# Kernel tuning notes

Measured on AMD Instinct MI355X. Metric: run time of the kernel, lower is better.

Reference implementation:

```python
import jax, jax.numpy as jnp
import numpy as np

EMBED_DIM = 1024
SEQ_LEN = 2048
BATCH = 4


def setup_inputs() -> dict:
    key = jax.random.key(0)
    kx, kq, kk, kv = jax.random.split(key, 4)
    scale = 1.0 / np.sqrt(EMBED_DIM)
    x = jax.random.normal(kx, (BATCH, SEQ_LEN, EMBED_DIM), dtype=jnp.float32)
    # nn.Linear weights are [out, in]; stored transposed-application here
    W_query = jax.random.normal(kq, (EMBED_DIM, EMBED_DIM), dtype=jnp.float32) * scale
    W_key = jax.random.normal(kk, (EMBED_DIM, EMBED_DIM), dtype=jnp.float32) * scale
    W_value = jax.random.normal(kv, (EMBED_DIM, EMBED_DIM), dtype=jnp.float32) * scale
    return {"x": x, "W_query": W_query, "W_key": W_key, "W_value": W_value}


def reference(x, W_query, W_key, W_value):
    # x: [B, S, D]; W_*: [D_out, D_in] (torch nn.Linear layout -> y = x @ W.T)
    B, S, D = x.shape
    q = jnp.einsum("bsd,ed->bse", x, W_query)
    k = jnp.einsum("bsd,ed->bse", x, W_key)
    v = jnp.einsum("bsd,ed->bse", x, W_value)
    scores = jnp.einsum("bqd,bkd->bqk", q, k)  # [B, S, S]
    causal = jnp.triu(jnp.ones((S, S), dtype=bool), k=1)  # True above diagonal
    scores = jnp.where(causal, -jnp.inf, scores)
    weights = jax.nn.softmax(scores / jnp.sqrt(jnp.asarray(D, x.dtype)), axis=-1)
    return jnp.einsum("bqk,bkd->bqd", weights, v)
```

## Files before the change

### kernel.cpp

```cpp
#include <hip/hip_runtime.h>
#include <stdint.h>

typedef __bf16 bf16_t;
typedef __bf16 bf16x8 __attribute__((ext_vector_type(8)));
typedef float  f32x4  __attribute__((ext_vector_type(4)));

#define AS1 __attribute__((address_space(1)))
#define AS3 __attribute__((address_space(3)))

__device__ __forceinline__ void gld_lds16(const bf16_t* g, void* s) {
  __builtin_amdgcn_global_load_lds((const AS1 uint32_t*)g, (AS3 uint32_t*)s, 16, 0, 0);
}

__global__ __launch_bounds__(256) void convert_all_kernel(
    const float* __restrict__ X,  const float* __restrict__ Wq,
    const float* __restrict__ Wk, const float* __restrict__ Wv,
    bf16_t* __restrict__ Xc, bf16_t* __restrict__ Wqc,
    bf16_t* __restrict__ Wkc, bf16_t* __restrict__ Wvc) {
  const int blk = blockIdx.x;
  const float* src; bf16_t* dst; int base;
  if (blk < 4096)      { src = X;  dst = Xc;  base = 0;    }
  else if (blk < 4608) { src = Wq; dst = Wqc; base = 4096; }
  else if (blk < 5120) { src = Wk; dst = Wkc; base = 4608; }
  else                 { src = Wv; dst = Wvc; base = 5120; }
  const int i = ((blk - base) * 256 + threadIdx.x) * 8;
  const float4 a = ((const float4*)(src + i))[0];
  const float4 b = ((const float4*)(src + i))[1];
  bf16x8 v;
  v[0] = (bf16_t)a.x; v[1] = (bf16_t)a.y; v[2] = (bf16_t)a.z; v[3] = (bf16_t)a.w;
  v[4] = (bf16_t)b.x; v[5] = (bf16_t)b.y; v[6] = (bf16_t)b.z; v[7] = (bf16_t)b.w;
  *(bf16x8*)(dst + i) = v;
}

__device__ __forceinline__ void gemm_bt_core(
    const bf16_t* __restrict__ A, int lda,
    const bf16_t* __restrict__ B, int ldb,
    int m0, int n0, int kBeg, int kEnd,
    bf16_t* As, bf16_t* Bs, f32x4 acc[4][4])
{
  const int tid  = threadIdx.x;
  const int lane = tid & 63;
  const int wave = tid >> 6;
  const int wm = (wave >> 1) * 64;
  const int wn = (wave & 1) * 64;
  const int fr = lane & 15;
  const int ck = lane >> 4;

  const int off0 = wave * 2048 + lane * 16;
  const int row0 = wave * 32 + (lane >> 2);
  const int row1 = row0 + 16;
  const int kg   = ((lane & 3) ^ ((row0 >> 1) & 3)) * 8;

  int aoff[4], boff[4];
#pragma unroll
  for (int i = 0; i < 4; ++i) {
    const int ra = wm + i * 16 + fr;
    const int rb = wn + i * 16 + fr;
    aoff[i] = ra * 64 + ((ck ^ ((ra >> 1) & 3)) * 16);
    boff[i] = rb * 64 + ((ck ^ ((rb >> 1) & 3)) * 16);
  }

  for (int kt = kBeg; kt < kEnd; kt += 32) {
    __syncthreads();
    gld_lds16(A + (size_t)(m0 + row0) * lda + kt + kg, (char*)As + off0);
    gld_lds16(A + (size_t)(m0 + row1) * lda + kt + kg, (char*)As + off0 + 1024);
    gld_lds16(B + (size_t)(n0 + row0) * ldb + kt + kg, (char*)Bs + off0);
    gld_lds16(B + (size_t)(n0 + row1) * ldb + kt + kg, (char*)Bs + off0 + 1024);
    __syncthreads();

    bf16x8 af[4], bfv[4];
#pragma unroll
    for (int mi = 0; mi < 4; ++mi)
      af[mi] = *(const bf16x8*)((char*)As + aoff[mi]);
#pragma unroll
    for (int ni = 0; ni < 4; ++ni)
      bfv[ni] = *(const bf16x8*)((char*)Bs + boff[ni]);
#pragma unroll
    for (int mi = 0; mi < 4; ++mi)
#pragma unroll
      for (int ni = 0; ni < 4; ++ni)
        acc[mi][ni] = __builtin_amdgcn_mfma_f32_16x16x32_bf16(
            af[mi], bfv[ni], acc[mi][ni], 0, 0, 0);
  }
}

__global__ __launch_bounds__(256) void qkv_kernel(
    const bf16_t* __restrict__ X,
    const bf16_t* __restrict__ Wq, const bf16_t* __restrict__ Wk,
    const bf16_t* __restrict__ Wv,
    bf16_t* __restrict__ Q, bf16_t* __restrict__ K, bf16_t* __restrict__ V)
{
  __shared__ bf16_t As[128 * 32];
  __shared__ bf16_t Bs[128 * 32];
  const int m0 = blockIdx.x * 128;
  const int n0 = blockIdx.y * 128;
  const int z  = blockIdx.z;
  const bf16_t* W = (z == 0) ? Wq : (z == 1) ? Wk : Wv;
  bf16_t* Out     = (z == 0) ? Q  : (z == 1) ? K  : V;

  f32x4 acc[4][4] = {};
  gemm_bt_core(X, 1024, W, 1024, m0, n0, 0, 1024, As, Bs, acc);

  const int lane = threadIdx.x & 63;
  const int wave = threadIdx.x >> 6;
  const int wm = (wave >> 1) * 64, wn = (wave & 1) * 64;
#pragma unroll
  for (int mi = 0; mi < 4; ++mi)
#pragma unroll
    for (int r = 0; r < 4; ++r) {
      const int row = m0 + wm + mi * 16 + (lane >> 4) * 4 + r;
#pragma unroll
      for (int ni = 0; ni < 4; ++ni) {
        const int col = n0 + wn + ni * 16 + (lane & 15);
        Out[(size_t)row * 1024 + col] = (bf16_t)acc[mi][ni][r];
      }
    }
}

__global__ __launch_bounds__(256) void vt_kernel(
    const bf16_t* __restrict__ V, bf16_t* __restrict__ Vt)
{
  __shared__ bf16_t t[64][66];
  const int b  = blockIdx.z;
  const int s0 = blockIdx.x * 64;
  const int d0 = blockIdx.y * 64;
  const bf16_t* Vb = V  + (size_t)b * 2048 * 1024;
  bf16_t* Vtb      = Vt + (size_t)b * 1024 * 2048;
  const int c = threadIdx.x & 63, r4 = threadIdx.x >> 6;
#pragma unroll
  for (int i = 0; i < 16; ++i) {
    const int r = r4 + i * 4;
    t[r][c] = Vb[(size_t)(s0 + r) * 1024 + d0 + c];
  }
  __syncthreads();
#pragma unroll
  for (int i = 0; i < 16; ++i) {
    const int r = r4 + i * 4;
    Vtb[(size_t)(d0 + r) * 2048 + s0 + c] = t[c][r];
  }
}

__global__ __launch_bounds__(256) void scores_exp_kernel(
    const bf16_t* __restrict__ Q, const bf16_t* __restrict__ K,
    bf16_t* __restrict__ P, float* __restrict__ partials)
{
  const int kt = blockIdx.x;
  const int mt = blockIdx.y;
  if (kt > mt) return;
  const int m0 = mt * 128;
  const int n0 = kt * 128;
  __shared__ bf16_t As[128 * 32];
  __shared__ bf16_t Bs[128 * 32];
  __shared__ float rowsum[2][128];
  const int batch = blockIdx.z;
  const bf16_t* Qb = Q + (size_t)batch * 2048 * 1024;
  const bf16_t* Kb = K + (size_t)batch * 2048 * 1024;
  bf16_t* Pb = P + (size_t)batch * 2048 * 2048;
  float* lp  = partials + ((size_t)batch * 16 + kt) * 2048;

  f32x4 acc[4][4] = {};
  gemm_bt_core(Qb, 1024, Kb, 1024, m0, n0, 0, 1024, As, Bs, acc);

  const int lane = threadIdx.x & 63;
  const int wave = threadIdx.x >> 6;
  const int wm = (wave >> 1) * 64, wn = (wave & 1) * 64;
  const float c = 0.04508422f;
#pragma unroll
  for (int mi = 0; mi < 4; ++mi)
#pragma unroll
    for (int r = 0; r < 4; ++r) {
      const int lrow = wm + mi * 16 + (lane >> 4) * 4 + r;
      const int row  = m0 + lrow;
      float rs = 0.f;
#pragma unroll
      for (int ni = 0; ni < 4; ++ni) {
        const int col = n0 + wn + ni * 16 + (lane & 15);
        float p = exp2f(acc[mi][ni][r] * c);
        if (col > row) p = 0.f;
        const bf16_t pb = (bf16_t)p;
        Pb[(size_t)row * 2048 + col] = pb;
        rs += (float)pb;
      }
      rs += __shfl_xor(rs, 1);
      rs += __shfl_xor(rs, 2);
      rs += __shfl_xor(rs, 4);
      rs += __shfl_xor(rs, 8);
      if ((lane & 15) == 0) rowsum[wave & 1][lrow] = rs;
    }
  __syncthreads();
  if (threadIdx.x < 128)
    lp[m0 + threadIdx.x] = rowsum[0][threadIdx.x] + rowsum[1][threadIdx.x];
}

__global__ __launch_bounds__(256) void lsum_kernel(
    const float* __restrict__ partials, float* __restrict__ Linv)
{
  const int id  = blockIdx.x * 256 + threadIdx.x;
  const int z   = id >> 11;
  const int row = id & 2047;
  const float* lp = partials + (size_t)z * 16 * 2048;
  const int tmax = row >> 7;
  float l = 0.f;
  for (int kt = 0; kt <= tmax; ++kt) l += lp[kt * 2048 + row];
  Linv[id] = 1.f / l;
}

__global__ __launch_bounds__(256) void pv_kernel(
    const bf16_t* __restrict__ P, const bf16_t* __restrict__ Vt,
    const float* __restrict__ Linv, float* __restrict__ out)
{
  __shared__ bf16_t As[128 * 32];
  __shared__ bf16_t Bs[128 * 32];
  const int zb = blockIdx.z;
  const int mt = ((zb >> 1) & 1) ? (15 - blockIdx.y) : blockIdx.y;
  const int m0 = mt * 128;
  const int n0 = blockIdx.x * 128;
  const bf16_t* Pb  = P  + (size_t)zb * 2048 * 2048;
  const bf16_t* Vtb = Vt + (size_t)zb * 1024 * 2048;
  const float* li = Linv + (size_t)zb * 2048;
  float* ob = out + (size_t)zb * 2048 * 1024;

  f32x4 acc[4][4] = {};
  gemm_bt_core(Pb, 2048, Vtb, 2048, m0, n0, 0, m0 + 128, As, Bs, acc);

  const int lane = threadIdx.x & 63;
  const int wave = threadIdx.x >> 6;
  const int wm = (wave >> 1) * 64, wn = (wave & 1) * 64;
#pragma unroll
  for (int mi = 0; mi < 4; ++mi)
#pragma unroll
    for (int r = 0; r < 4; ++r) {
      const int row = m0 + wm + mi * 16 + (lane >> 4) * 4 + r;
      const float inv = li[row];
#pragma unroll
      for (int ni = 0; ni < 4; ++ni) {
        const int col = n0 + wn + ni * 16 + (lane & 15);
        ob[(size_t)row * 1024 + col] = acc[mi][ni][r] * inv;
      }
    }
}

extern "C" void kernel_launch(void* const* d_in, const int* in_sizes, int n_in,
                              void* d_out, int out_size, void* d_ws, size_t ws_size,
                              hipStream_t stream) {
  const float* X  = (const float*)d_in[0];
  const float* Wq = (const float*)d_in[1];
  const float* Wk = (const float*)d_in[2];
  const float* Wv = (const float*)d_in[3];
  float* out = (float*)d_out;
  char* ws = (char*)d_ws;

  const size_t MB = 1024 * 1024;
  bf16_t* Q    = (bf16_t*)(ws + 0 * MB);
  bf16_t* K    = (bf16_t*)(ws + 16 * MB);
  bf16_t* V    = (bf16_t*)(ws + 32 * MB);
  bf16_t* Xc   = (bf16_t*)(ws + 48 * MB);
  bf16_t* Wqc  = (bf16_t*)(ws + 64 * MB);
  bf16_t* Wkc  = (bf16_t*)(ws + 66 * MB);
  bf16_t* Wvc  = (bf16_t*)(ws + 68 * MB);
  bf16_t* P    = (bf16_t*)(ws + 48 * MB);
  bf16_t* Vt   = (bf16_t*)(ws + 0 * MB);
  float*  Lp   = (float*)(ws + 80 * MB);
  float*  Linv = (float*)(ws + 80 * MB + 512 * 1024);

  convert_all_kernel<<<dim3(5632), 256, 0, stream>>>(X, Wq, Wk, Wv, Xc, Wqc, Wkc, Wvc);
  qkv_kernel<<<dim3(64, 8, 3), 256, 0, stream>>>(Xc, Wqc, Wkc, Wvc, Q, K, V);
  scores_exp_kernel<<<dim3(16, 16, 4), 256, 0, stream>>>(Q, K, P, Lp);
  lsum_kernel<<<dim3(32), 256, 0, stream>>>(Lp, Linv);
  vt_kernel<<<dim3(32, 16, 4), 256, 0, stream>>>(V, Vt);
  pv_kernel<<<dim3(8, 16, 4), 256, 0, stream>>>(P, Vt, Linv, out);
}
```

Baseline: 265.2 us.

## Double GEMM K-tile to 64 and fuse V transpose into QKV epilogue

The shared GEMM core now stages 64-wide K tiles with an 8-way XOR swizzle, halving the number of barrier pairs per K loop and issuing more MFMAs per synchronization. The QKV kernel writes V directly in transposed layout through an LDS staging buffer, which removes the separate vt_kernel launch and its extra read and write of V. This doubles the LDS footprint per block, which may reduce occupancy, and adds extra barriers in the V epilogue.

```diff
diff --git a/kernel.cpp b/kernel.cpp
--- a/kernel.cpp
+++ b/kernel.cpp
@@ -2,6 +2,7 @@
 #include <stdint.h>
 
 typedef __bf16 bf16_t;
+typedef __bf16 bf16x4 __attribute__((ext_vector_type(4)));
 typedef __bf16 bf16x8 __attribute__((ext_vector_type(8)));
 typedef float  f32x4  __attribute__((ext_vector_type(4)));
 
@@ -38,49 +39,62 @@
     int m0, int n0, int kBeg, int kEnd,
     bf16_t* As, bf16_t* Bs, f32x4 acc[4][4])
 {
-  const int tid  = threadIdx.x;
-  const int lane = tid & 63;
-  const int wave = tid >> 6;
+  const int lane = threadIdx.x & 63;
+  const int wave = threadIdx.x >> 6;
   const int wm = (wave >> 1) * 64;
   const int wn = (wave & 1) * 64;
   const int fr = lane & 15;
   const int ck = lane >> 4;
 
-  const int off0 = wave * 2048 + lane * 16;
-  const int row0 = wave * 32 + (lane >> 2);
-  const int row1 = row0 + 16;
-  const int kg   = ((lane & 3) ^ ((row0 >> 1) & 3)) * 8;
-
-  int aoff[4], boff[4];
+  const int srow = lane >> 3;
+  const int sch  = lane & 7;
+
+  int grow[4], kg[4], dst[4];
+#pragma unroll
+  for (int j = 0; j < 4; ++j) {
+    const int r = wave * 32 + j * 8 + srow;
+    grow[j] = r;
+    kg[j]   = (sch ^ (r & 7)) * 8;
+    dst[j]  = r * 128 + sch * 16;
+  }
+
+  int aoff[4][2], boff[4][2];
 #pragma unroll
   for (int i = 0; i < 4; ++i) {
     const int ra = wm + i * 16 + fr;
     const int rb = wn + i * 16 + fr;
-    aoff[i] = ra * 64 + ((ck ^ ((ra >> 1) & 3)) * 16);
-    boff[i] = rb * 64 + ((ck ^ ((rb >> 1) & 3)) * 16);
-  }
-
-  for (int kt = kBeg; kt < kEnd; kt += 32) {
+#pragma unroll
+    for (int kh = 0; kh < 2; ++kh) {
+      aoff[i][kh] = ra * 128 + (((kh * 4 + ck) ^ (ra & 7)) * 16);
+      boff[i][kh] = rb * 128 + (((kh * 4 + ck) ^ (rb & 7)) * 16);
+    }
+  }
+
+  for (int kt = kBeg; kt < kEnd; kt += 64) {
     __syncthreads();
-    gld_lds16(A + (size_t)(m0 + row0) * lda + kt + kg, (char*)As + off0);
-    gld_lds16(A + (size_t)(m0 + row1) * lda + kt + kg, (char*)As + off0 + 1024);
-    gld_lds16(B + (size_t)(n0 + row0) * ldb + kt + kg, (char*)Bs + off0);
-    gld_lds16(B + (size_t)(n0 + row1) * ldb + kt + kg, (char*)Bs + off0 + 1024);
+#pragma unroll
+    for (int j = 0; j < 4; ++j) {
+      gld_lds16(A + (size_t)(m0 + grow[j]) * lda + kt + kg[j], (char*)As + dst[j]);
+      gld_lds16(B + (size_t)(n0 + grow[j]) * ldb + kt + kg[j], (char*)Bs + dst[j]);
+    }
     __syncthreads();
 
-    bf16x8 af[4], bfv[4];
-#pragma unroll
-    for (int mi = 0; mi < 4; ++mi)
-      af[mi] = *(const bf16x8*)((char*)As + aoff[mi]);
-#pragma unroll
-    for (int ni = 0; ni < 4; ++ni)
-      bfv[ni] = *(const bf16x8*)((char*)Bs + boff[ni]);
-#pragma unroll
-    for (int mi = 0; mi < 4; ++mi)
-#pragma unroll
-      for (int ni = 0; ni < 4; ++ni)
-        acc[mi][ni] = __builtin_amdgcn_mfma_f32_16x16x32_bf16(
-            af[mi], bfv[ni], acc[mi][ni], 0, 0, 0);
+    bf16x8 af[4][2], bfv[4][2];
+#pragma unroll
+    for (int i = 0; i < 4; ++i)
+#pragma unroll
+      for (int kh = 0; kh < 2; ++kh) {
+        af[i][kh]  = *(const bf16x8*)((char*)As + aoff[i][kh]);
+        bfv[i][kh] = *(const bf16x8*)((char*)Bs + boff[i][kh]);
+      }
+#pragma unroll
+    for (int kh = 0; kh < 2; ++kh)
+#pragma unroll
+      for (int mi = 0; mi < 4; ++mi)
+#pragma unroll
+        for (int ni = 0; ni < 4; ++ni)
+          acc[mi][ni] = __builtin_amdgcn_mfma_f32_16x16x32_bf16(
+              af[mi][kh], bfv[ni][kh], acc[mi][ni], 0, 0, 0);
   }
 }
 
@@ -88,15 +102,15 @@
     const bf16_t* __restrict__ X,
     const bf16_t* __restrict__ Wq, const bf16_t* __restrict__ Wk,
     const bf16_t* __restrict__ Wv,
-    bf16_t* __restrict__ Q, bf16_t* __restrict__ K, bf16_t* __restrict__ V)
-{
-  __shared__ bf16_t As[128 * 32];
-  __shared__ bf16_t Bs[128 * 32];
+    bf16_t* __restrict__ Q, bf16_t* __restrict__ K, bf16_t* __restrict__ Vt)
+{
+  __shared__ bf16_t smem[2 * 128 * 64];
+  bf16_t* As = smem;
+  bf16_t* Bs = smem + 128 * 64;
   const int m0 = blockIdx.x * 128;
   const int n0 = blockIdx.y * 128;
   const int z  = blockIdx.z;
   const bf16_t* W = (z == 0) ? Wq : (z == 1) ? Wk : Wv;
-  bf16_t* Out     = (z == 0) ? Q  : (z == 1) ? K  : V;
 
   f32x4 acc[4][4] = {};
   gemm_bt_core(X, 1024, W, 1024, m0, n0, 0, 1024, As, Bs, acc);
@@ -104,39 +118,51 @@
   const int lane = threadIdx.x & 63;
   const int wave = threadIdx.x >> 6;
   const int wm = (wave >> 1) * 64, wn = (wave & 1) * 64;
-#pragma unroll
-  for (int mi = 0; mi < 4; ++mi)
-#pragma unroll
-    for (int r = 0; r < 4; ++r) {
-      const int row = m0 + wm + mi * 16 + (lane >> 4) * 4 + r;
-#pragma unroll
-      for (int ni = 0; ni < 4; ++ni) {
-        const int col = n0 + wn + ni * 16 + (lane & 15);
-        Out[(size_t)row * 1024 + col] = (bf16_t)acc[mi][ni][r];
-      }
-    }
-}
-
-__global__ __launch_bounds__(256) void vt_kernel(
-    const bf16_t* __restrict__ V, bf16_t* __restrict__ Vt)
-{
-  __shared__ bf16_t t[64][66];
-  const int b  = blockIdx.z;
-  const int s0 = blockIdx.x * 64;
-  const int d0 = blockIdx.y * 64;
-  const bf16_t* Vb = V  + (size_t)b * 2048 * 1024;
-  bf16_t* Vtb      = Vt + (size_t)b * 1024 * 2048;
-  const int c = threadIdx.x & 63, r4 = threadIdx.x >> 6;
-#pragma unroll
-  for (int i = 0; i < 16; ++i) {
-    const int r = r4 + i * 4;
-    t[r][c] = Vb[(size_t)(s0 + r) * 1024 + d0 + c];
-  }
-  __syncthreads();
-#pragma unroll
-  for (int i = 0; i < 16; ++i) {
-    const int r = r4 + i * 4;
-    Vtb[(size_t)(d0 + r) * 2048 + s0 + c] = t[c][r];
+
+  if (z < 2) {
+    bf16_t* Out = z ? K : Q;
+#pragma unroll
+    for (int mi = 0; mi < 4; ++mi)
+#pragma unroll
+      for (int r = 0; r < 4; ++r) {
+        const int row = m0 + wm + mi * 16 + (lane >> 4) * 4 + r;
+#pragma unroll
+        for (int ni = 0; ni < 4; ++ni) {
+          const int col = n0 + wn + ni * 16 + (lane & 15);
+          Out[(size_t)row * 1024 + col] = (bf16_t)acc[mi][ni][r];
+        }
+      }
+  } else {
+    const int b  = m0 >> 11;
+    const int s0 = m0 & 2047;
+    bf16_t* Vtb = Vt + (size_t)b * 1024 * 2048;
+    bf16_t (*t)[136] = (bf16_t(*)[136])smem;
+#pragma unroll
+    for (int h = 0; h < 2; ++h) {
+      __syncthreads();
+      if ((wave & 1) == h) {
+#pragma unroll
+        for (int mi = 0; mi < 4; ++mi)
+#pragma unroll
+          for (int ni = 0; ni < 4; ++ni) {
+            const int c   = ni * 16 + (lane & 15);
+            const int row = wm + mi * 16 + (lane >> 4) * 4;
+            bf16x4 v;
+            v[0] = (bf16_t)acc[mi][ni][0]; v[1] = (bf16_t)acc[mi][ni][1];
+            v[2] = (bf16_t)acc[mi][ni][2]; v[3] = (bf16_t)acc[mi][ni][3];
+            *(bf16x4*)&t[c][row] = v;
+          }
+      }
+      __syncthreads();
+#pragma unroll
+      for (int i = 0; i < 4; ++i) {
+        const int u  = threadIdx.x + 256 * i;
+        const int d  = u >> 4;
+        const int ch = u & 15;
+        bf16x8 vv = *(const bf16x8*)&t[d][ch * 8];
+        *(bf16x8*)(Vtb + (size_t)(n0 + h * 64 + d) * 2048 + s0 + ch * 8) = vv;
+      }
+    }
   }
 }
 
@@ -149,9 +175,10 @@
   if (kt > mt) return;
   const int m0 = mt * 128;
   const int n0 = kt * 128;
-  __shared__ bf16_t As[128 * 32];
-  __shared__ bf16_t Bs[128 * 32];
+  __shared__ bf16_t smem[2 * 128 * 64];
   __shared__ float rowsum[2][128];
+  bf16_t* As = smem;
+  bf16_t* Bs = smem + 128 * 64;
   const int batch = blockIdx.z;
   const bf16_t* Qb = Q + (size_t)batch * 2048 * 1024;
   const bf16_t* Kb = K + (size_t)batch * 2048 * 1024;
@@ -209,8 +236,9 @@
     const bf16_t* __restrict__ P, const bf16_t* __restrict__ Vt,
     const float* __restrict__ Linv, float* __restrict__ out)
 {
-  __shared__ bf16_t As[128 * 32];
-  __shared__ bf16_t Bs[128 * 32];
+  __shared__ bf16_t smem[2 * 128 * 64];
+  bf16_t* As = smem;
+  bf16_t* Bs = smem + 128 * 64;
   const int zb = blockIdx.z;
   const int mt = ((zb >> 1) & 1) ? (15 - blockIdx.y) : blockIdx.y;
   const int m0 = mt * 128;
@@ -253,20 +281,18 @@
   const size_t MB = 1024 * 1024;
   bf16_t* Q    = (bf16_t*)(ws + 0 * MB);
   bf16_t* K    = (bf16_t*)(ws + 16 * MB);
-  bf16_t* V    = (bf16_t*)(ws + 32 * MB);
+  bf16_t* Vt   = (bf16_t*)(ws + 32 * MB);
   bf16_t* Xc   = (bf16_t*)(ws + 48 * MB);
   bf16_t* Wqc  = (bf16_t*)(ws + 64 * MB);
   bf16_t* Wkc  = (bf16_t*)(ws + 66 * MB);
   bf16_t* Wvc  = (bf16_t*)(ws + 68 * MB);
   bf16_t* P    = (bf16_t*)(ws + 48 * MB);
-  bf16_t* Vt   = (bf16_t*)(ws + 0 * MB);
   float*  Lp   = (float*)(ws + 80 * MB);
   float*  Linv = (float*)(ws + 80 * MB + 512 * 1024);
 
   convert_all_kernel<<<dim3(5632), 256, 0, stream>>>(X, Wq, Wk, Wv, Xc, Wqc, Wkc, Wvc);
-  qkv_kernel<<<dim3(64, 8, 3), 256, 0, stream>>>(Xc, Wqc, Wkc, Wvc, Q, K, V);
+  qkv_kernel<<<dim3(64, 8, 3), 256, 0, stream>>>(Xc, Wqc, Wkc, Wvc, Q, K, Vt);
   scores_exp_kernel<<<dim3(16, 16, 4), 256, 0, stream>>>(Q, K, P, Lp);
   lsum_kernel<<<dim3(32), 256, 0, stream>>>(Lp, Linv);
-  vt_kernel<<<dim3(32, 16, 4), 256, 0, stream>>>(V, Vt);
   pv_kernel<<<dim3(8, 16, 4), 256, 0, stream>>>(P, Vt, Linv, out);
 }
```

After: 251.5 us. 5.2% less time.
